# Performance work log

Measured on AMD Instinct MI355X. Metric: run time of the kernel, lower is better.

## Reference

```python
import jax, jax.numpy as jnp
import numpy as np

N = 50000      # nodes
E = 600000     # edges
D_IN = 128
D_H = 128
D_OUT = 64
HEADS = 2
NEG_SLOPE = 0.2  # PyG GATConv default leaky_relu slope
BN_EPS = 1e-5


def setup_inputs() -> dict:
    key = jax.random.key(0)
    ks = jax.random.split(key, 24)
    w = lambda i, shape: (jax.random.normal(ks[i], shape, jnp.float32) * 0.1)
    return {
        "x": jax.random.normal(ks[0], (N, D_IN), jnp.float32),
        "edge_index": jax.random.randint(ks[1], (2, E), 0, N, jnp.int64),
        "W_gcn1": w(2, (D_IN, D_H)),
        "b_gcn1": jnp.zeros((D_H,), jnp.float32),
        "bn1_gamma": jax.random.uniform(ks[3], (D_H,), jnp.float32, 0.5, 1.5),
        "bn1_beta": w(4, (D_H,)),
        "bn1_mean": w(5, (D_H,)),
        "bn1_var": jax.random.uniform(ks[6], (D_H,), jnp.float32, 0.5, 1.5),
        "W_gat1": w(7, (D_H, HEADS * D_H)),
        "a_src1": w(8, (HEADS, D_H)),
        "a_dst1": w(9, (HEADS, D_H)),
        "b_gat1": jnp.zeros((D_H,), jnp.float32),
        "W_gcn2": w(10, (D_H, D_H)),
        "b_gcn2": jnp.zeros((D_H,), jnp.float32),
        "bn2_gamma": jax.random.uniform(ks[11], (D_H,), jnp.float32, 0.5, 1.5),
        "bn2_beta": w(12, (D_H,)),
        "bn2_mean": w(13, (D_H,)),
        "bn2_var": jax.random.uniform(ks[14], (D_H,), jnp.float32, 0.5, 1.5),
        "W_gat2": w(15, (D_H, HEADS * D_OUT)),
        "a_src2": w(16, (HEADS, D_OUT)),
        "a_dst2": w(17, (HEADS, D_OUT)),
        "b_gat2": jnp.zeros((D_OUT,), jnp.float32),
    }


def _add_self_loops(edge_index):
    loop = jnp.arange(N, dtype=edge_index.dtype)
    src = jnp.concatenate([edge_index[0], loop])
    dst = jnp.concatenate([edge_index[1], loop])
    return src, dst


def _gcn(x, edge_index, W, b):
    # PyG GCNConv: add self-loops, symmetric D^-1/2 (A+I) D^-1/2 normalization
    src, dst = _add_self_loops(edge_index)
    deg = jax.ops.segment_sum(jnp.ones_like(dst, x.dtype), dst, num_segments=N)
    dinv = jax.lax.rsqrt(jnp.maximum(deg, 1.0))  # deg >= 1 with self-loops
    norm = dinv[src] * dinv[dst]                 # [E+N]
    h = x @ W                                    # [N, C]
    out = jax.ops.segment_sum(h[src] * norm[:, None], dst, num_segments=N)
    return out + b


def _gat(x, edge_index, W, a_src, a_dst, b, out_ch):
    # PyG GATConv (concat=False): per-head attention, segment softmax over dst,
    # mean across heads. Dropout off (eval mode).
    h = (x @ W).reshape(N, HEADS, out_ch)                 # [N, H, C]
    al_s = jnp.einsum('nhc,hc->nh', h, a_src)             # [N, H]
    al_d = jnp.einsum('nhc,hc->nh', h, a_dst)             # [N, H]
    src, dst = _add_self_loops(edge_index)
    e = al_s[src] + al_d[dst]                             # [E+N, H]
    e = jnp.where(e > 0, e, NEG_SLOPE * e)                # leaky_relu
    m = jax.ops.segment_max(e, dst, num_segments=N)       # [N, H]
    ex = jnp.exp(e - m[dst])
    denom = jax.ops.segment_sum(ex, dst, num_segments=N)  # [N, H]
    alpha = ex / denom[dst]                               # [E+N, H]
    out = jax.ops.segment_sum(h[src] * alpha[:, :, None], dst, num_segments=N)
    return out.mean(axis=1) + b                           # concat=False -> mean


def _bn_eval(x, gamma, beta, mean, var):
    return (x - mean) * jax.lax.rsqrt(var + BN_EPS) * gamma + beta


def reference(x, edge_index, W_gcn1, b_gcn1, bn1_gamma, bn1_beta, bn1_mean, bn1_var,
              W_gat1, a_src1, a_dst1, b_gat1, W_gcn2, b_gcn2,
              bn2_gamma, bn2_beta, bn2_mean, bn2_var,
              W_gat2, a_src2, a_dst2, b_gat2):
    h = _gcn(x, edge_index, W_gcn1, b_gcn1)
    h = jax.nn.relu(_bn_eval(h, bn1_gamma, bn1_beta, bn1_mean, bn1_var))
    h = jax.nn.relu(_gat(h, edge_index, W_gat1, a_src1, a_dst1, b_gat1, D_H))
    h = _gcn(h, edge_index, W_gcn2, b_gcn2)
    h = jax.nn.relu(_bn_eval(h, bn2_gamma, bn2_beta, bn2_mean, bn2_var))
    h = _gat(h, edge_index, W_gat2, a_src2, a_dst2, b_gat2, D_OUT)
    return jax.nn.log_softmax(h, axis=1)
```

## Files before the change

kernel.cpp:

```cpp
#include <hip/hip_runtime.h>
#include <hip/hip_bf16.h>

#define N_NODES 50000
#define N_EDGES 600000

typedef short bf16x8 __attribute__((ext_vector_type(8)));
typedef float f32x4 __attribute__((ext_vector_type(4)));

__device__ __forceinline__ float leaky(float e) { return fmaxf(e, 0.2f * e); }
__device__ __forceinline__ unsigned short f2b(float f) {
  __hip_bfloat16 h = __float2bfloat16(f);
  return *reinterpret_cast<unsigned short*>(&h);
}
__device__ __forceinline__ float blo(unsigned int u) { return __uint_as_float(u << 16); }
__device__ __forceinline__ float bhi(unsigned int u) { return __uint_as_float(u & 0xffff0000u); }

__global__ void k_convert(const int* __restrict__ e, int* __restrict__ deg,
                          int2* __restrict__ eord,
                          const float* __restrict__ W1, const float* __restrict__ WG1,
                          const float* __restrict__ W2, const float* __restrict__ WG2,
                          unsigned short* __restrict__ Wt1, unsigned short* __restrict__ WtG1,
                          unsigned short* __restrict__ Wt2, unsigned short* __restrict__ WtG2,
                          const float* b1, const float* g1, const float* be1, const float* m1,
                          const float* v1, const float* b2, const float* g2, const float* be2,
                          const float* m2, const float* v2, float* sc1, float* sh1,
                          float* sc2, float* sh2,
                          const float* as1, const float* ad1, const float* as2,
                          const float* ad2, float* was1, float* wad1, float* was2,
                          float* wad2) {
  __shared__ int sflag;
  int tid = threadIdx.x;
  if (tid < 64) {
    int idx = 1 + 2 * tid * 4096;
    int v = e[idx];
    unsigned long long nz = __ballot(v != 0);
    if (tid == 0) sflag = (nz == 0ULL) ? 1 : 0;
  }
  __syncthreads();
  int f = sflag;
  int i = blockIdx.x * 256 + tid;
  if (i < N_EDGES) {
    int s, d;
    if (f) { s = e[2 * i]; d = e[2 * (N_EDGES + i)]; }
    else   { s = e[i];     d = e[N_EDGES + i]; }
    int pos = atomicAdd(&deg[d], 1);
    eord[i] = make_int2(s, (d << 16) | pos);
  }
  if (i < 16384) {
    int k = i >> 7, c = i & 127;
    Wt1[c * 128 + k] = f2b(W1[i]);
  } else if (i < 49152) {
    int l = i - 16384;
    int k = l >> 8, c8 = l & 255;
    int head = c8 >> 7, cc = c8 & 127;
    WtG1[cc * 256 + head * 128 + k] = f2b(WG1[l]);
  } else if (i < 65536) {
    int l = i - 49152;
    int k = l >> 7, c = l & 127;
    Wt2[c * 128 + k] = f2b(W2[l]);
  } else if (i < 81920) {
    int l = i - 65536;
    int k = l >> 7, c = l & 127;
    WtG2[c * 128 + k] = f2b(WG2[l]);
  } else if (i < 82048) {
    int c = i - 81920;
    float s = g1[c] * rsqrtf(v1[c] + 1e-5f);
    sc1[c] = s;
    sh1[c] = (b1[c] - m1[c]) * s + be1[c];
  } else if (i < 82176) {
    int c = i - 82048;
    float s = g2[c] * rsqrtf(v2[c] + 1e-5f);
    sc2[c] = s;
    sh2[c] = (b2[c] - m2[c]) * s + be2[c];
  } else if (i < 82688) {
    int j = i - 82176;
    int k = j & 127;
    int vec = j >> 7;
    const float* Wr = (vec < 2) ? (WG1 + k * 256) : (WG2 + k * 128);
    const float* av = (vec == 0) ? as1 : (vec == 1) ? ad1 : (vec == 2) ? as2 : ad2;
    float* op = (vec == 0) ? was1 : (vec == 1) ? wad1 : (vec == 2) ? was2 : wad2;
    int hl = (vec < 2) ? 128 : 64;
    float s0 = 0.f, s1 = 0.f;
    for (int c = 0; c < hl; c += 4) {
      float4 wv = *(const float4*)(Wr + c);
      float4 a4 = *(const float4*)(av + c);
      s0 += wv.x * a4.x + wv.y * a4.y + wv.z * a4.z + wv.w * a4.w;
    }
    for (int c = 0; c < hl; c += 4) {
      float4 wv = *(const float4*)(Wr + hl + c);
      float4 a4 = *(const float4*)(av + hl + c);
      s1 += wv.x * a4.x + wv.y * a4.y + wv.z * a4.z + wv.w * a4.w;
    }
    op[2 * k] = s0;
    op[2 * k + 1] = s1;
  }
}

__global__ void k_offsets(const int* __restrict__ deg, int* __restrict__ gbase,
                          int* __restrict__ roff, float* __restrict__ dinv) {
  __shared__ int s[256];
  __shared__ int base;
  int t = threadIdx.x;
  int i = blockIdx.x * 256 + t;
  int v = (i < N_NODES) ? deg[i] : 0;
  s[t] = v;
  __syncthreads();
  for (int o = 1; o < 256; o <<= 1) {
    int x = (t >= o) ? s[t - o] : 0;
    __syncthreads();
    s[t] += x;
    __syncthreads();
  }
  if (t == 255) base = atomicAdd(gbase, s[255]);
  __syncthreads();
  int off = base + s[t] - v;
  if (i < N_NODES) {
    roff[i] = off;
    dinv[i] = rsqrtf((float)v + 1.f);
  }
}
__global__ void k_fill(const int2* __restrict__ eord, const int* __restrict__ roff,
                       int2* __restrict__ aen, const float* __restrict__ dinv) {
  int i = blockIdx.x * 256 + threadIdx.x;
  if (i < N_EDGES) {
    int2 ep = eord[i];
    int s = ep.x;
    int d = ((unsigned)ep.y) >> 16;
    int pos = ep.y & 0xffff;
    aen[roff[d] + pos] = make_int2(s, __float_as_int(dinv[s]));
  }
}

__global__ __launch_bounds__(256, 4) void gemm_mfma(const float* __restrict__ X,
                                                    const unsigned short* __restrict__ Wt,
                                                    unsigned short* __restrict__ Hb) {
  __shared__ __align__(16) short smem[64 * 136];
  int tid = threadIdx.x;
  int row0 = blockIdx.x * 64;
  for (int i = tid; i < 2048; i += 256) {
    int r = i >> 5;
    int k4 = (i & 31) * 4;
    int row = row0 + r;
    float4 v = make_float4(0.f, 0.f, 0.f, 0.f);
    if (row < N_NODES) v = *(const float4*)(X + (size_t)row * 128 + k4);
    uint2 p;
    p.x = (unsigned int)f2b(v.x) | ((unsigned int)f2b(v.y) << 16);
    p.y = (unsigned int)f2b(v.z) | ((unsigned int)f2b(v.w) << 16);
    *(uint2*)&smem[r * 136 + k4] = p;
  }
  int wave = tid >> 6, lane = tid & 63;
  int m = lane & 15, quad = lane >> 4;
  int c0 = wave * 32;
  bf16x8 b[2][4];
#pragma unroll
  for (int ct = 0; ct < 2; ++ct) {
    const unsigned short* wp = Wt + (size_t)(c0 + ct * 16 + m) * 128 + quad * 8;
#pragma unroll
    for (int kk = 0; kk < 4; ++kk) b[ct][kk] = *(const bf16x8*)(wp + kk * 32);
  }
  __syncthreads();
  f32x4 acc[4][2];
#pragma unroll
  for (int rt = 0; rt < 4; ++rt)
#pragma unroll
    for (int ct = 0; ct < 2; ++ct) acc[rt][ct] = (f32x4){0.f, 0.f, 0.f, 0.f};
#pragma unroll
  for (int rt = 0; rt < 4; ++rt) {
    bf16x8 a[4];
#pragma unroll
    for (int kk = 0; kk < 4; ++kk)
      a[kk] = *(const bf16x8*)&smem[(rt * 16 + m) * 136 + kk * 32 + quad * 8];
#pragma unroll
    for (int ct = 0; ct < 2; ++ct)
#pragma unroll
      for (int kk = 0; kk < 4; ++kk)
        acc[rt][ct] = __builtin_amdgcn_mfma_f32_16x16x32_bf16(a[kk], b[ct][kk], acc[rt][ct], 0, 0, 0);
  }
  __syncthreads();
#pragma unroll
  for (int rt = 0; rt < 4; ++rt)
#pragma unroll
    for (int ct = 0; ct < 2; ++ct)
#pragma unroll
      for (int reg = 0; reg < 4; ++reg)
        smem[(rt * 16 + quad * 4 + reg) * 128 + c0 + ct * 16 + m] = (short)f2b(acc[rt][ct][reg]);
  __syncthreads();
  for (int i = tid; i < 1024; i += 256) {
    int row = row0 + (i >> 4);
    if (row < N_NODES)
      *(uint4*)((char*)Hb + (size_t)row0 * 256 + (size_t)i * 16) =
          *(uint4*)((char*)smem + (size_t)i * 16);
  }
}

__global__ __launch_bounds__(256, 4) void gemm_k256(const unsigned short* __restrict__ Q,
                                                    const unsigned short* __restrict__ Wt,
                                                    const float* __restrict__ bias,
                                                    unsigned short* __restrict__ G) {
  __shared__ __align__(16) short smem[64 * 136];
  int tid = threadIdx.x;
  int row0 = blockIdx.x * 64;
  int wave = tid >> 6, lane = tid & 63;
  int m = lane & 15, quad = lane >> 4;
  int c0 = wave * 32;
  f32x4 acc[4][2];
#pragma unroll
  for (int rt = 0; rt < 4; ++rt)
#pragma unroll
    for (int ct = 0; ct < 2; ++ct) acc[rt][ct] = (f32x4){0.f, 0.f, 0.f, 0.f};
#pragma unroll
  for (int half = 0; half < 2; ++half) {
    if (half) __syncthreads();
    for (int i = tid; i < 2048; i += 256) {
      int r = i >> 5;
      int k4 = (i & 31) * 4;
      int row = row0 + r;
      uint2 p = make_uint2(0u, 0u);
      if (row < N_NODES) p = *(const uint2*)(Q + (size_t)row * 256 + half * 128 + k4);
      *(uint2*)&smem[r * 136 + k4] = p;
    }
    bf16x8 b[2][4];
#pragma unroll
    for (int ct = 0; ct < 2; ++ct) {
      const unsigned short* wp =
          Wt + (size_t)(c0 + ct * 16 + m) * 256 + half * 128 + quad * 8;
#pragma unroll
      for (int kk = 0; kk < 4; ++kk) b[ct][kk] = *(const bf16x8*)(wp + kk * 32);
    }
    __syncthreads();
#pragma unroll
    for (int rt = 0; rt < 4; ++rt) {
      bf16x8 a[4];
#pragma unroll
      for (int kk = 0; kk < 4; ++kk)
        a[kk] = *(const bf16x8*)&smem[(rt * 16 + m) * 136 + kk * 32 + quad * 8];
#pragma unroll
      for (int ct = 0; ct < 2; ++ct)
#pragma unroll
        for (int kk = 0; kk < 4; ++kk)
          acc[rt][ct] =
              __builtin_amdgcn_mfma_f32_16x16x32_bf16(a[kk], b[ct][kk], acc[rt][ct], 0, 0, 0);
    }
  }
  __syncthreads();
  float bv[2];
#pragma unroll
  for (int ct = 0; ct < 2; ++ct) bv[ct] = bias[c0 + ct * 16 + m];
#pragma unroll
  for (int rt = 0; rt < 4; ++rt)
#pragma unroll
    for (int ct = 0; ct < 2; ++ct)
#pragma unroll
      for (int reg = 0; reg < 4; ++reg)
        smem[(rt * 16 + quad * 4 + reg) * 128 + c0 + ct * 16 + m] =
            (short)f2b(fmaxf(acc[rt][ct][reg] + bv[ct], 0.f));
  __syncthreads();
  for (int i = tid; i < 1024; i += 256) {
    int row = row0 + (i >> 4);
    if (row < N_NODES)
      *(uint4*)((char*)G + (size_t)row0 * 256 + (size_t)i * 16) =
          *(uint4*)((char*)smem + (size_t)i * 16);
  }
}

__global__ __launch_bounds__(256, 4) void gemm_gcn2_gat2(
    const unsigned short* __restrict__ AG, const unsigned short* __restrict__ Wt2,
    const float* __restrict__ sc, const float* __restrict__ sh,
    const unsigned short* __restrict__ WtG2,
    const float* __restrict__ was, const float* __restrict__ wad,
    float* __restrict__ als, float* __restrict__ ald,
    unsigned short* __restrict__ Q2) {
  __shared__ __align__(16) short smA[64 * 136];
  __shared__ __align__(16) short smB[64 * 136];
  int tid = threadIdx.x;
  int row0 = blockIdx.x * 64;
  for (int i = tid; i < 1024; i += 256) {
    int r = i >> 4;
    int k8 = (i & 15) * 8;
    int row = row0 + r;
    uint4 p = make_uint4(0u, 0u, 0u, 0u);
    if (row < N_NODES) p = *(const uint4*)(AG + (size_t)row * 128 + k8);
    *(uint4*)&smA[r * 136 + k8] = p;
  }
  int wave = tid >> 6, lane = tid & 63;
  int m = lane & 15, quad = lane >> 4;
  int c0 = wave * 32;
  bf16x8 b1[2][4];
#pragma unroll
  for (int ct = 0; ct < 2; ++ct) {
    const unsigned short* wp = Wt2 + (size_t)(c0 + ct * 16 + m) * 128 + quad * 8;
#pragma unroll
    for (int kk = 0; kk < 4; ++kk) b1[ct][kk] = *(const bf16x8*)(wp + kk * 32);
  }
  __syncthreads();
  f32x4 acc[4][2];
#pragma unroll
  for (int rt = 0; rt < 4; ++rt)
#pragma unroll
    for (int ct = 0; ct < 2; ++ct) acc[rt][ct] = (f32x4){0.f, 0.f, 0.f, 0.f};
#pragma unroll
  for (int rt = 0; rt < 4; ++rt) {
    bf16x8 a[4];
#pragma unroll
    for (int kk = 0; kk < 4; ++kk)
      a[kk] = *(const bf16x8*)&smA[(rt * 16 + m) * 136 + kk * 32 + quad * 8];
#pragma unroll
    for (int ct = 0; ct < 2; ++ct)
#pragma unroll
      for (int kk = 0; kk < 4; ++kk)
        acc[rt][ct] = __builtin_amdgcn_mfma_f32_16x16x32_bf16(a[kk], b1[ct][kk], acc[rt][ct], 0, 0, 0);
  }
  float scv[2], shv[2];
#pragma unroll
  for (int ct = 0; ct < 2; ++ct) {
    scv[ct] = sc[c0 + ct * 16 + m];
    shv[ct] = sh[c0 + ct * 16 + m];
  }
#pragma unroll
  for (int rt = 0; rt < 4; ++rt)
#pragma unroll
    for (int ct = 0; ct < 2; ++ct)
#pragma unroll
      for (int reg = 0; reg < 4; ++reg)
        smB[(rt * 16 + quad * 4 + reg) * 136 + c0 + ct * 16 + m] =
            (short)f2b(fmaxf(fmaf(acc[rt][ct][reg], scv[ct], shv[ct]), 0.f));
  __syncthreads();
  bf16x8 b2[2][4];
#pragma unroll
  for (int ct = 0; ct < 2; ++ct) {
    const unsigned short* wp = WtG2 + (size_t)(c0 + ct * 16 + m) * 128 + quad * 8;
#pragma unroll
    for (int kk = 0; kk < 4; ++kk) b2[ct][kk] = *(const bf16x8*)(wp + kk * 32);
  }
  f32x4 acc2[4][2];
#pragma unroll
  for (int rt = 0; rt < 4; ++rt)
#pragma unroll
    for (int ct = 0; ct < 2; ++ct) acc2[rt][ct] = (f32x4){0.f, 0.f, 0.f, 0.f};
#pragma unroll
  for (int rt = 0; rt < 4; ++rt) {
    bf16x8 a[4];
#pragma unroll
    for (int kk = 0; kk < 4; ++kk)
      a[kk] = *(const bf16x8*)&smB[(rt * 16 + m) * 136 + kk * 32 + quad * 8];
#pragma unroll
    for (int ct = 0; ct < 2; ++ct)
#pragma unroll
      for (int kk = 0; kk < 4; ++kk)
        acc2[rt][ct] = __builtin_amdgcn_mfma_f32_16x16x32_bf16(a[kk], b2[ct][kk], acc2[rt][ct], 0, 0, 0);
  }
  {
    int rloc = wave * 16 + (lane >> 2);
    int k0 = (lane & 3) * 32;
    float s0 = 0.f, s1 = 0.f, d0 = 0.f, d1 = 0.f;
#pragma unroll
    for (int c = 0; c < 32; c += 2) {
      unsigned u = *(const unsigned*)&smB[rloc * 136 + k0 + c];
      float x0 = blo(u), x1 = bhi(u);
      float4 ws4 = *(const float4*)(was + 2 * (k0 + c));
      float4 wd4 = *(const float4*)(wad + 2 * (k0 + c));
      s0 = fmaf(x0, ws4.x, s0); s1 = fmaf(x0, ws4.y, s1);
      s0 = fmaf(x1, ws4.z, s0); s1 = fmaf(x1, ws4.w, s1);
      d0 = fmaf(x0, wd4.x, d0); d1 = fmaf(x0, wd4.y, d1);
      d0 = fmaf(x1, wd4.z, d0); d1 = fmaf(x1, wd4.w, d1);
    }
#pragma unroll
    for (int mask = 1; mask <= 2; mask <<= 1) {
      s0 += __shfl_xor(s0, mask, 64);
      s1 += __shfl_xor(s1, mask, 64);
      d0 += __shfl_xor(d0, mask, 64);
      d1 += __shfl_xor(d1, mask, 64);
    }
    int row = row0 + rloc;
    if ((lane & 3) == 0 && row < N_NODES) {
      *(float2*)(als + 2 * row) = make_float2(s0, s1);
      *(float2*)(ald + 2 * row) = make_float2(d0, d1);
    }
  }
#pragma unroll
  for (int rt = 0; rt < 4; ++rt)
#pragma unroll
    for (int ct = 0; ct < 2; ++ct)
#pragma unroll
      for (int reg = 0; reg < 4; ++reg)
        smA[(rt * 16 + quad * 4 + reg) * 128 + c0 + ct * 16 + m] =
            (short)f2b(acc2[rt][ct][reg]);
  __syncthreads();
  for (int i = tid; i < 1024; i += 256) {
    int row = row0 + (i >> 4);
    if (row < N_NODES)
      *(uint4*)((char*)Q2 + (size_t)row0 * 256 + (size_t)i * 16) =
          *(uint4*)((char*)smA + (size_t)i * 16);
  }
}

template <int MODE>
__global__ __launch_bounds__(256) void gcn_pull(const unsigned short* __restrict__ Hb,
                                                const int2* __restrict__ aen,
                                                const int* __restrict__ roff,
                                                const int* __restrict__ deg,
                                                const float* __restrict__ dinv,
                                                const float* __restrict__ sc,
                                                const float* __restrict__ sh,
                                                const float* __restrict__ was,
                                                const float* __restrict__ wad,
                                                float* __restrict__ als,
                                                float* __restrict__ ald,
                                                unsigned short* __restrict__ out) {
  int wv = (blockIdx.x * 256 + threadIdx.x) >> 6;
  int lane = threadIdx.x & 63;
  int q4 = lane >> 4, l16 = lane & 15;
  int qb = lane & 48, l7 = lane & 7;
  int i = 4 * wv + q4;
  if (i >= N_NODES) return;
  int off = roff[i], end = off + deg[i];
  float di = dinv[i];
  uint4 u = *(const uint4*)((const char*)Hb + (unsigned)i * 256u + l16 * 16u);
  float a0 = blo(u.x) * di, a1 = bhi(u.x) * di;
  float a2 = blo(u.y) * di, a3 = bhi(u.y) * di;
  float a4 = blo(u.z) * di, a5 = bhi(u.z) * di;
  float a6 = blo(u.w) * di, a7 = bhi(u.w) * di;
  int j = off;
  int nfull = (end - off) >> 3;
  int2 ae = make_int2(i, 0);
  if (l7 < end - j) ae = aen[j + l7];
  for (int t = 0; t < nfull; ++t) {
    int ss[8];
#pragma unroll
    for (int k = 0; k < 8; ++k) ss[k] = __shfl(ae.x, qb + k, 64);
    float ww[8];
#pragma unroll
    for (int k = 0; k < 8; ++k) ww[k] = __shfl(__int_as_float(ae.y), qb + k, 64);
    uint4 vv[8];
#pragma unroll
    for (int k = 0; k < 8; ++k)
      vv[k] = *(const uint4*)((const char*)Hb + (unsigned)ss[k] * 256u + l16 * 16u);
    j += 8;
    if (l7 < end - j) ae = aen[j + l7];
#pragma unroll
    for (int k = 0; k < 8; ++k) {
      a0 = fmaf(blo(vv[k].x), ww[k], a0); a1 = fmaf(bhi(vv[k].x), ww[k], a1);
      a2 = fmaf(blo(vv[k].y), ww[k], a2); a3 = fmaf(bhi(vv[k].y), ww[k], a3);
      a4 = fmaf(blo(vv[k].z), ww[k], a4); a5 = fmaf(bhi(vv[k].z), ww[k], a5);
      a6 = fmaf(blo(vv[k].w), ww[k], a6); a7 = fmaf(bhi(vv[k].w), ww[k], a7);
    }
  }
  int rem = end - j;
  if (rem) {
    int ss[8];
#pragma unroll
    for (int k = 0; k < 8; ++k) ss[k] = __shfl(ae.x, qb + k, 64);
    float ww[8];
#pragma unroll
    for (int k = 0; k < 8; ++k) ww[k] = __shfl(__int_as_float(ae.y), qb + k, 64);
    uint4 vv[8];
#pragma unroll
    for (int k = 0; k < 8; ++k)
      if (k < rem)
        vv[k] = *(const uint4*)((const char*)Hb + (unsigned)ss[k] * 256u + l16 * 16u);
#pragma unroll
    for (int k = 0; k < 8; ++k)
      if (k < rem) {
        a0 = fmaf(blo(vv[k].x), ww[k], a0); a1 = fmaf(bhi(vv[k].x), ww[k], a1);
        a2 = fmaf(blo(vv[k].y), ww[k], a2); a3 = fmaf(bhi(vv[k].y), ww[k], a3);
        a4 = fmaf(blo(vv[k].z), ww[k], a4); a5 = fmaf(bhi(vv[k].z), ww[k], a5);
        a6 = fmaf(blo(vv[k].w), ww[k], a6); a7 = fmaf(bhi(vv[k].w), ww[k], a7);
      }
  }
  if constexpr (MODE == 1) {
    uint4 pw;
    pw.x = (unsigned int)f2b(a0 * di) | ((unsigned int)f2b(a1 * di) << 16);
    pw.y = (unsigned int)f2b(a2 * di) | ((unsigned int)f2b(a3 * di) << 16);
    pw.z = (unsigned int)f2b(a4 * di) | ((unsigned int)f2b(a5 * di) << 16);
    pw.w = (unsigned int)f2b(a6 * di) | ((unsigned int)f2b(a7 * di) << 16);
    *(uint4*)(out + (size_t)i * 128 + l16 * 8) = pw;
  } else {
    int c0 = l16 * 8;
    float4 sca = *(const float4*)(sc + c0), scb = *(const float4*)(sc + c0 + 4);
    float4 sha = *(const float4*)(sh + c0), shb = *(const float4*)(sh + c0 + 4);
    float t0 = fmaxf(fmaf(a0 * di, sca.x, sha.x), 0.f);
    float t1 = fmaxf(fmaf(a1 * di, sca.y, sha.y), 0.f);
    float t2 = fmaxf(fmaf(a2 * di, sca.z, sha.z), 0.f);
    float t3 = fmaxf(fmaf(a3 * di, sca.w, sha.w), 0.f);
    float t4 = fmaxf(fmaf(a4 * di, scb.x, shb.x), 0.f);
    float t5 = fmaxf(fmaf(a5 * di, scb.y, shb.y), 0.f);
    float t6 = fmaxf(fmaf(a6 * di, scb.z, shb.z), 0.f);
    float t7 = fmaxf(fmaf(a7 * di, scb.w, shb.w), 0.f);
    float4 w0 = *(const float4*)(was + 2 * c0);
    float4 w1 = *(const float4*)(was + 2 * c0 + 4);
    float4 w2 = *(const float4*)(was + 2 * c0 + 8);
    float4 w3 = *(const float4*)(was + 2 * c0 + 12);
    float sl0 = t0 * w0.x + t1 * w0.z + t2 * w1.x + t3 * w1.z +
                t4 * w2.x + t5 * w2.z + t6 * w3.x + t7 * w3.z;
    float sl1 = t0 * w0.y + t1 * w0.w + t2 * w1.y + t3 * w1.w +
                t4 * w2.y + t5 * w2.w + t6 * w3.y + t7 * w3.w;
    w0 = *(const float4*)(wad + 2 * c0);
    w1 = *(const float4*)(wad + 2 * c0 + 4);
    w2 = *(const float4*)(wad + 2 * c0 + 8);
    w3 = *(const float4*)(wad + 2 * c0 + 12);
    float dl0 = t0 * w0.x + t1 * w0.z + t2 * w1.x + t3 * w1.z +
                t4 * w2.x + t5 * w2.z + t6 * w3.x + t7 * w3.z;
    float dl1 = t0 * w0.y + t1 * w0.w + t2 * w1.y + t3 * w1.w +
                t4 * w2.y + t5 * w2.w + t6 * w3.y + t7 * w3.w;
#pragma unroll
    for (int mask = 1; mask <= 8; mask <<= 1) {
      sl0 += __shfl_xor(sl0, mask, 64);
      sl1 += __shfl_xor(sl1, mask, 64);
      dl0 += __shfl_xor(dl0, mask, 64);
      dl1 += __shfl_xor(dl1, mask, 64);
    }
    if (l16 == 0) {
      *(float2*)(als + 2 * i) = make_float2(sl0, sl1);
      *(float2*)(ald + 2 * i) = make_float2(dl0, dl1);
    }
    uint4 pw;
    pw.x = (unsigned int)f2b(t0) | ((unsigned int)f2b(t1) << 16);
    pw.y = (unsigned int)f2b(t2) | ((unsigned int)f2b(t3) << 16);
    pw.z = (unsigned int)f2b(t4) | ((unsigned int)f2b(t5) << 16);
    pw.w = (unsigned int)f2b(t6) | ((unsigned int)f2b(t7) << 16);
    *(uint4*)(out + (size_t)i * 128 + l16 * 8) = pw;
  }
}

__global__ __launch_bounds__(256) void gat1_pull(const unsigned short* __restrict__ P,
                                                 const int2* __restrict__ aen,
                                                 const int* __restrict__ roff,
                                                 const int* __restrict__ deg,
                                                 const float* __restrict__ als,
                                                 const float* __restrict__ ald,
                                                 unsigned short* __restrict__ Q) {
  int wv = (blockIdx.x * 256 + threadIdx.x) >> 6;
  int lane = threadIdx.x & 63;
  int q4 = lane >> 4, l16 = lane & 15;
  int qb = lane & 48, l7 = lane & 7;
  int i = 4 * wv + q4;
  if (i >= N_NODES) return;
  int off = roff[i], end = off + deg[i];
  float2 dif = *(const float2*)(ald + 2 * i);
  float p0 = 0.f, p1 = 0.f;
  float g0 = 0.f, g1 = 0.f, g2 = 0.f, g3 = 0.f,
        g4 = 0.f, g5 = 0.f, g6 = 0.f, g7 = 0.f;
  float h0 = 0.f, h1 = 0.f, h2 = 0.f, h3 = 0.f,
        h4 = 0.f, h5 = 0.f, h6 = 0.f, h7 = 0.f;
  int j = off;
  int nfull = (end - off) >> 3;
  int2 ae = make_int2(i, 0);
  float2 av = make_float2(-1e30f, -1e30f);
  if (l7 < end - j) {
    ae = aen[j + l7];
    av = *(const float2*)(als + 2 * ae.x);
  }
  for (int t = 0; t < nfull; ++t) {
    int ss[8];
#pragma unroll
    for (int k = 0; k < 8; ++k) ss[k] = __shfl(ae.x, qb + k, 64);
    uint4 vv[8];
#pragma unroll
    for (int k = 0; k < 8; ++k)
      vv[k] = *(const uint4*)((const char*)P + (unsigned)ss[k] * 256u + l16 * 16u);
    float q0 = __expf(leaky(av.x + dif.x));
    float q1 = __expf(leaky(av.y + dif.y));
    j += 8;
    if (l7 < end - j) {
      ae = aen[j + l7];
      av = *(const float2*)(als + 2 * ae.x);
    }
#pragma unroll
    for (int k = 0; k < 8; ++k) {
      float b0 = __shfl(q0, qb + k, 64);
      float b1 = __shfl(q1, qb + k, 64);
      p0 += b0; p1 += b1;
      float c0 = blo(vv[k].x), c1 = bhi(vv[k].x);
      float c2 = blo(vv[k].y), c3 = bhi(vv[k].y);
      float c4 = blo(vv[k].z), c5 = bhi(vv[k].z);
      float c6 = blo(vv[k].w), c7 = bhi(vv[k].w);
      g0 = fmaf(b0, c0, g0); h0 = fmaf(b1, c0, h0);
      g1 = fmaf(b0, c1, g1); h1 = fmaf(b1, c1, h1);
      g2 = fmaf(b0, c2, g2); h2 = fmaf(b1, c2, h2);
      g3 = fmaf(b0, c3, g3); h3 = fmaf(b1, c3, h3);
      g4 = fmaf(b0, c4, g4); h4 = fmaf(b1, c4, h4);
      g5 = fmaf(b0, c5, g5); h5 = fmaf(b1, c5, h5);
      g6 = fmaf(b0, c6, g6); h6 = fmaf(b1, c6, h6);
      g7 = fmaf(b0, c7, g7); h7 = fmaf(b1, c7, h7);
    }
  }
  int rem = end - j;
  if (rem) {
    int ss[8];
#pragma unroll
    for (int k = 0; k < 8; ++k) ss[k] = __shfl(ae.x, qb + k, 64);
    uint4 vv[8];
#pragma unroll
    for (int k = 0; k < 8; ++k)
      if (k < rem)
        vv[k] = *(const uint4*)((const char*)P + (unsigned)ss[k] * 256u + l16 * 16u);
    float q0 = __expf(leaky(av.x + dif.x));
    float q1 = __expf(leaky(av.y + dif.y));
#pragma unroll
    for (int k = 0; k < 8; ++k)
      if (k < rem) {
        float b0 = __shfl(q0, qb + k, 64);
        float b1 = __shfl(q1, qb + k, 64);
        p0 += b0; p1 += b1;
        float c0 = blo(vv[k].x), c1 = bhi(vv[k].x);
        float c2 = blo(vv[k].y), c3 = bhi(vv[k].y);
        float c4 = blo(vv[k].z), c5 = bhi(vv[k].z);
        float c6 = blo(vv[k].w), c7 = bhi(vv[k].w);
        g0 = fmaf(b0, c0, g0); h0 = fmaf(b1, c0, h0);
        g1 = fmaf(b0, c1, g1); h1 = fmaf(b1, c1, h1);
        g2 = fmaf(b0, c2, g2); h2 = fmaf(b1, c2, h2);
        g3 = fmaf(b0, c3, g3); h3 = fmaf(b1, c3, h3);
        g4 = fmaf(b0, c4, g4); h4 = fmaf(b1, c4, h4);
        g5 = fmaf(b0, c5, g5); h5 = fmaf(b1, c5, h5);
        g6 = fmaf(b0, c6, g6); h6 = fmaf(b1, c6, h6);
        g7 = fmaf(b0, c7, g7); h7 = fmaf(b1, c7, h7);
      }
  }
  float2 ai = *(const float2*)(als + 2 * i);
  float es0 = __expf(leaky(ai.x + dif.x));
  float es1 = __expf(leaky(ai.y + dif.y));
  float r0 = 0.5f / (p0 + es0);
  float r1 = 0.5f / (p1 + es1);
  uint4 u = *(const uint4*)((const char*)P + (unsigned)i * 256u + l16 * 16u);
  float c0 = blo(u.x), c1 = bhi(u.x), c2 = blo(u.y), c3 = bhi(u.y);
  float c4 = blo(u.z), c5 = bhi(u.z), c6 = blo(u.w), c7 = bhi(u.w);
  g0 = (g0 + es0 * c0) * r0; g1 = (g1 + es0 * c1) * r0;
  g2 = (g2 + es0 * c2) * r0; g3 = (g3 + es0 * c3) * r0;
  g4 = (g4 + es0 * c4) * r0; g5 = (g5 + es0 * c5) * r0;
  g6 = (g6 + es0 * c6) * r0; g7 = (g7 + es0 * c7) * r0;
  h0 = (h0 + es1 * c0) * r1; h1 = (h1 + es1 * c1) * r1;
  h2 = (h2 + es1 * c2) * r1; h3 = (h3 + es1 * c3) * r1;
  h4 = (h4 + es1 * c4) * r1; h5 = (h5 + es1 * c5) * r1;
  h6 = (h6 + es1 * c6) * r1; h7 = (h7 + es1 * c7) * r1;
  uint4 pw;
  pw.x = (unsigned int)f2b(g0) | ((unsigned int)f2b(g1) << 16);
  pw.y = (unsigned int)f2b(g2) | ((unsigned int)f2b(g3) << 16);
  pw.z = (unsigned int)f2b(g4) | ((unsigned int)f2b(g5) << 16);
  pw.w = (unsigned int)f2b(g6) | ((unsigned int)f2b(g7) << 16);
  *(uint4*)(Q + (size_t)i * 256 + l16 * 8) = pw;
  pw.x = (unsigned int)f2b(h0) | ((unsigned int)f2b(h1) << 16);
  pw.y = (unsigned int)f2b(h2) | ((unsigned int)f2b(h3) << 16);
  pw.z = (unsigned int)f2b(h4) | ((unsigned int)f2b(h5) << 16);
  pw.w = (unsigned int)f2b(h6) | ((unsigned int)f2b(h7) << 16);
  *(uint4*)(Q + (size_t)i * 256 + 128 + l16 * 8) = pw;
}

__global__ __launch_bounds__(256) void gat_pull64_lsm(const unsigned short* __restrict__ Hb,
                                                      const int2* __restrict__ aen,
                                                      const int* __restrict__ roff,
                                                      const int* __restrict__ deg,
                                                      const float* __restrict__ als,
                                                      const float* __restrict__ ald,
                                                      const float* __restrict__ bias,
                                                      float* __restrict__ out) {
  int wv = (blockIdx.x * 256 + threadIdx.x) >> 6;
  int lane = threadIdx.x & 63;
  int q4 = lane >> 4, l16 = lane & 15;
  int qb = lane & 48, l7 = lane & 7;
  int hh = l16 >> 3, p8 = l16 & 7;
  int i = 4 * wv + q4;
  if (i >= N_NODES) return;
  int off = roff[i], end = off + deg[i];
  unsigned cb2 = (unsigned)(hh * 64 + 8 * p8) * 2u;
  float2 dd = *(const float2*)(ald + 2 * i);
  float p = 0.f;
  float acc0 = 0.f, acc1 = 0.f, acc2 = 0.f, acc3 = 0.f;
  float acc4 = 0.f, acc5 = 0.f, acc6 = 0.f, acc7 = 0.f;
  int j = off;
  int nfull = (end - off) >> 3;
  int2 ae = make_int2(i, 0);
  float2 av = make_float2(-1e30f, -1e30f);
  if (l7 < end - j) {
    ae = aen[j + l7];
    av = *(const float2*)(als + 2 * ae.x);
  }
  for (int t = 0; t < nfull; ++t) {
    int ss[8];
#pragma unroll
    for (int k = 0; k < 8; ++k) ss[k] = __shfl(ae.x, qb + k, 64);
    uint4 vv[8];
#pragma unroll
    for (int k = 0; k < 8; ++k)
      vv[k] = *(const uint4*)((const char*)Hb + (unsigned)ss[k] * 256u + cb2);
    float q0 = __expf(leaky(av.x + dd.x));
    float q1 = __expf(leaky(av.y + dd.y));
    j += 8;
    if (l7 < end - j) {
      ae = aen[j + l7];
      av = *(const float2*)(als + 2 * ae.x);
    }
#pragma unroll
    for (int k = 0; k < 8; ++k) {
      float b0 = __shfl(q0, qb + k, 64);
      float b1 = __shfl(q1, qb + k, 64);
      float q = hh ? b1 : b0;
      p += q;
      acc0 = fmaf(q, blo(vv[k].x), acc0); acc1 = fmaf(q, bhi(vv[k].x), acc1);
      acc2 = fmaf(q, blo(vv[k].y), acc2); acc3 = fmaf(q, bhi(vv[k].y), acc3);
      acc4 = fmaf(q, blo(vv[k].z), acc4); acc5 = fmaf(q, bhi(vv[k].z), acc5);
      acc6 = fmaf(q, blo(vv[k].w), acc6); acc7 = fmaf(q, bhi(vv[k].w), acc7);
    }
  }
  int rem = end - j;
  if (rem) {
    int ss[8];
#pragma unroll
    for (int k = 0; k < 8; ++k) ss[k] = __shfl(ae.x, qb + k, 64);
    uint4 vv[8];
#pragma unroll
    for (int k = 0; k < 8; ++k)
      if (k < rem)
        vv[k] = *(const uint4*)((const char*)Hb + (unsigned)ss[k] * 256u + cb2);
    float q0 = __expf(leaky(av.x + dd.x));
    float q1 = __expf(leaky(av.y + dd.y));
#pragma unroll
    for (int k = 0; k < 8; ++k)
      if (k < rem) {
        float b0 = __shfl(q0, qb + k, 64);
        float b1 = __shfl(q1, qb + k, 64);
        float q = hh ? b1 : b0;
        p += q;
        acc0 = fmaf(q, blo(vv[k].x), acc0); acc1 = fmaf(q, bhi(vv[k].x), acc1);
        acc2 = fmaf(q, blo(vv[k].y), acc2); acc3 = fmaf(q, bhi(vv[k].y), acc3);
        acc4 = fmaf(q, blo(vv[k].z), acc4); acc5 = fmaf(q, bhi(vv[k].z), acc5);
        acc6 = fmaf(q, blo(vv[k].w), acc6); acc7 = fmaf(q, bhi(vv[k].w), acc7);
      }
  }
  float2 ai = *(const float2*)(als + 2 * i);
  float axs = hh ? ai.y : ai.x;
  float dh = hh ? dd.y : dd.x;
  float es = __expf(leaky(axs + dh));
  float rsel = 0.5f / (p + es);
  uint4 u = *(const uint4*)((const char*)Hb + (unsigned)i * 256u + cb2);
  acc0 = (acc0 + es * blo(u.x)) * rsel; acc1 = (acc1 + es * bhi(u.x)) * rsel;
  acc2 = (acc2 + es * blo(u.y)) * rsel; acc3 = (acc3 + es * bhi(u.y)) * rsel;
  acc4 = (acc4 + es * blo(u.z)) * rsel; acc5 = (acc5 + es * bhi(u.z)) * rsel;
  acc6 = (acc6 + es * blo(u.w)) * rsel; acc7 = (acc7 + es * bhi(u.w)) * rsel;
  acc0 += __shfl_xor(acc0, 8, 64); acc1 += __shfl_xor(acc1, 8, 64);
  acc2 += __shfl_xor(acc2, 8, 64); acc3 += __shfl_xor(acc3, 8, 64);
  acc4 += __shfl_xor(acc4, 8, 64); acc5 += __shfl_xor(acc5, 8, 64);
  acc6 += __shfl_xor(acc6, 8, 64); acc7 += __shfl_xor(acc7, 8, 64);
  float4 b0 = *(const float4*)(bias + 8 * p8);
  float4 b1 = *(const float4*)(bias + 8 * p8 + 4);
  float v0 = acc0 + b0.x, v1 = acc1 + b0.y, v2 = acc2 + b0.z, v3 = acc3 + b0.w;
  float v4 = acc4 + b1.x, v5 = acc5 + b1.y, v6 = acc6 + b1.z, v7 = acc7 + b1.w;
  float mv = fmaxf(fmaxf(fmaxf(v0, v1), fmaxf(v2, v3)),
                   fmaxf(fmaxf(v4, v5), fmaxf(v6, v7)));
#pragma unroll
  for (int mm = 4; mm > 0; mm >>= 1) mv = fmaxf(mv, __shfl_xor(mv, mm, 64));
  float sv = __expf(v0 - mv) + __expf(v1 - mv) + __expf(v2 - mv) + __expf(v3 - mv) +
             __expf(v4 - mv) + __expf(v5 - mv) + __expf(v6 - mv) + __expf(v7 - mv);
#pragma unroll
  for (int mm = 4; mm > 0; mm >>= 1) sv += __shfl_xor(sv, mm, 64);
  float ls = mv + __logf(sv);
  if (hh == 0) {
    *(float4*)(out + (size_t)i * 64 + 8 * p8) =
        make_float4(v0 - ls, v1 - ls, v2 - ls, v3 - ls);
    *(float4*)(out + (size_t)i * 64 + 8 * p8 + 4) =
        make_float4(v4 - ls, v5 - ls, v6 - ls, v7 - ls);
  }
}

extern "C" void kernel_launch(void* const* d_in, const int* in_sizes, int n_in, void* d_out,
                              int out_size, void* d_ws, size_t ws_size, hipStream_t stream) {
  const float* x      = (const float*)d_in[0];
  const int* eidx     = (const int*)d_in[1];
  const float* W_gcn1 = (const float*)d_in[2];
  const float* b_gcn1 = (const float*)d_in[3];
  const float* bn1_g  = (const float*)d_in[4];
  const float* bn1_b  = (const float*)d_in[5];
  const float* bn1_m  = (const float*)d_in[6];
  const float* bn1_v  = (const float*)d_in[7];
  const float* W_gat1 = (const float*)d_in[8];
  const float* a_src1 = (const float*)d_in[9];
  const float* a_dst1 = (const float*)d_in[10];
  const float* b_gat1 = (const float*)d_in[11];
  const float* W_gcn2 = (const float*)d_in[12];
  const float* b_gcn2 = (const float*)d_in[13];
  const float* bn2_g  = (const float*)d_in[14];
  const float* bn2_b  = (const float*)d_in[15];
  const float* bn2_m  = (const float*)d_in[16];
  const float* bn2_v  = (const float*)d_in[17];
  const float* W_gat2 = (const float*)d_in[18];
  const float* a_src2 = (const float*)d_in[19];
  const float* a_dst2 = (const float*)d_in[20];
  const float* b_gat2 = (const float*)d_in[21];

  char* ws = (char*)d_ws;
  size_t o = 0;
  auto take = [&](size_t bytes) {
    char* p = ws + o;
    o = (o + bytes + 255) & ~(size_t)255;
    return p;
  };
  int* deg     = (int*)take((size_t)(N_NODES + 64) * 4);
  int* gbase   = deg + N_NODES;
  int* roff    = (int*)take((size_t)N_NODES * 4);
  int2* eord   = (int2*)take((size_t)N_EDGES * 8);
  int2* aen    = (int2*)take((size_t)N_EDGES * 8);
  float* dinv  = (float*)take((size_t)N_NODES * 4);
  float* als   = (float*)take((size_t)2 * N_NODES * 4);
  float* ald   = (float*)take((size_t)2 * N_NODES * 4);
  float* sc1   = (float*)take(128 * 4);
  float* sh1   = (float*)take(128 * 4);
  float* sc2   = (float*)take(128 * 4);
  float* sh2   = (float*)take(128 * 4);
  float* was1  = (float*)take(256 * 4);
  float* wad1  = (float*)take(256 * 4);
  float* was2  = (float*)take(256 * 4);
  float* wad2  = (float*)take(256 * 4);
  unsigned short* Wt1  = (unsigned short*)take((size_t)128 * 128 * 2);
  unsigned short* WtG1 = (unsigned short*)take((size_t)128 * 256 * 2);
  unsigned short* Wt2  = (unsigned short*)take((size_t)128 * 128 * 2);
  unsigned short* WtG2 = (unsigned short*)take((size_t)128 * 128 * 2);
  unsigned short* Hb   = (unsigned short*)take((size_t)N_NODES * 128 * 2);
  unsigned short* Pb   = (unsigned short*)take((size_t)N_NODES * 128 * 2);
  unsigned short* Qb   = (unsigned short*)take((size_t)N_NODES * 256 * 2);
  unsigned short* Gb   = (unsigned short*)take((size_t)N_NODES * 128 * 2);
  unsigned short* AGb  = (unsigned short*)take((size_t)N_NODES * 128 * 2);
  unsigned short* Q2b  = (unsigned short*)take((size_t)N_NODES * 128 * 2);
  (void)ws_size; (void)in_sizes; (void)n_in; (void)out_size;

  int eb = (N_EDGES + 255) / 256;
  int nb = (N_NODES + 255) / 256;
  int qb = ((N_NODES + 3) / 4 + 3) / 4;
  int gb = (N_NODES + 63) / 64;

  hipMemsetAsync(deg, 0, (size_t)(N_NODES + 1) * 4, stream);
  k_convert<<<eb, 256, 0, stream>>>(eidx, deg, eord, W_gcn1, W_gat1, W_gcn2, W_gat2,
                                    Wt1, WtG1, Wt2, WtG2, b_gcn1, bn1_g, bn1_b, bn1_m, bn1_v,
                                    b_gcn2, bn2_g, bn2_b, bn2_m, bn2_v, sc1, sh1, sc2, sh2,
                                    a_src1, a_dst1, a_src2, a_dst2, was1, wad1, was2, wad2);
  k_offsets<<<nb, 256, 0, stream>>>(deg, gbase, roff, dinv);
  k_fill<<<eb, 256, 0, stream>>>(eord, roff, aen, dinv);

  gemm_mfma<<<gb, 256, 0, stream>>>(x, Wt1, Hb);
  gcn_pull<0><<<qb, 256, 0, stream>>>(Hb, aen, roff, deg, dinv, sc1, sh1, was1, wad1,
                                      als, ald, Pb);
  gat1_pull<<<qb, 256, 0, stream>>>(Pb, aen, roff, deg, als, ald, Qb);
  gemm_k256<<<gb, 256, 0, stream>>>(Qb, WtG1, b_gat1, Gb);
  gcn_pull<1><<<qb, 256, 0, stream>>>(Gb, aen, roff, deg, dinv, nullptr, nullptr,
                                      nullptr, nullptr, nullptr, nullptr, AGb);
  gemm_gcn2_gat2<<<gb, 256, 0, stream>>>(AGb, Wt2, sc2, sh2, WtG2, was2, wad2,
                                         als, ald, Q2b);
  gat_pull64_lsm<<<qb, 256, 0, stream>>>(Q2b, aen, roff, deg, als, ald, b_gat2,
                                         (float*)d_out);
}
```

Measured before the change: 314.2 us.

## Fuse first GCN GEMM into edge conversion kernel and widen k256 tile loads

The first-layer X·W GEMM now runs as extra blocks of the edge/weight conversion kernel, reading and converting the fp32 W_gcn1 to bf16 directly in registers. This removes the separate Wt1 transpose buffer and one kernel launch, and lets the GEMM overlap with the degree-counting atomics. The WtG1 conversion range is remapped, and part of it is now written twice with identical values. Separately, the k256 GEMM stages its smem tile with 16-byte loads instead of 8-byte loads. The cost is strided, uncoalesced fp32 weight reads in every GEMM block and a larger combined grid.

New measurement: 305.7 us. 2.7% less time.

```diff
diff --git a/kernel.cpp b/kernel.cpp
--- a/kernel.cpp
+++ b/kernel.cpp
@@ -3,6 +3,7 @@
 
 #define N_NODES 50000
 #define N_EDGES 600000
+#define GEMM_BLOCKS 782
 
 typedef short bf16x8 __attribute__((ext_vector_type(8)));
 typedef float f32x4 __attribute__((ext_vector_type(4)));
@@ -15,21 +16,86 @@
 __device__ __forceinline__ float blo(unsigned int u) { return __uint_as_float(u << 16); }
 __device__ __forceinline__ float bhi(unsigned int u) { return __uint_as_float(u & 0xffff0000u); }
 
-__global__ void k_convert(const int* __restrict__ e, int* __restrict__ deg,
-                          int2* __restrict__ eord,
-                          const float* __restrict__ W1, const float* __restrict__ WG1,
-                          const float* __restrict__ W2, const float* __restrict__ WG2,
-                          unsigned short* __restrict__ Wt1, unsigned short* __restrict__ WtG1,
-                          unsigned short* __restrict__ Wt2, unsigned short* __restrict__ WtG2,
-                          const float* b1, const float* g1, const float* be1, const float* m1,
-                          const float* v1, const float* b2, const float* g2, const float* be2,
-                          const float* m2, const float* v2, float* sc1, float* sh1,
-                          float* sc2, float* sh2,
-                          const float* as1, const float* ad1, const float* as2,
-                          const float* ad2, float* was1, float* wad1, float* was2,
-                          float* wad2) {
+__global__ __launch_bounds__(256, 4) void k_convert_gemm(
+    const int* __restrict__ e, int* __restrict__ deg, int2* __restrict__ eord,
+    const float* __restrict__ X, unsigned short* __restrict__ Hb,
+    const float* __restrict__ W1, const float* __restrict__ WG1,
+    const float* __restrict__ W2, const float* __restrict__ WG2,
+    unsigned short* __restrict__ WtG1,
+    unsigned short* __restrict__ Wt2, unsigned short* __restrict__ WtG2,
+    const float* b1, const float* g1, const float* be1, const float* m1,
+    const float* v1, const float* b2, const float* g2, const float* be2,
+    const float* m2, const float* v2, float* sc1, float* sh1,
+    float* sc2, float* sh2,
+    const float* as1, const float* ad1, const float* as2,
+    const float* ad2, float* was1, float* wad1, float* was2, float* wad2) {
+  __shared__ __align__(16) short smem[64 * 136];
+  int tid = threadIdx.x;
+  if (blockIdx.x < GEMM_BLOCKS) {
+    int row0 = blockIdx.x * 64;
+    for (int i = tid; i < 2048; i += 256) {
+      int r = i >> 5;
+      int k4 = (i & 31) * 4;
+      int row = row0 + r;
+      float4 v = make_float4(0.f, 0.f, 0.f, 0.f);
+      if (row < N_NODES) v = *(const float4*)(X + (size_t)row * 128 + k4);
+      uint2 p;
+      p.x = (unsigned int)f2b(v.x) | ((unsigned int)f2b(v.y) << 16);
+      p.y = (unsigned int)f2b(v.z) | ((unsigned int)f2b(v.w) << 16);
+      *(uint2*)&smem[r * 136 + k4] = p;
+    }
+    int wave = tid >> 6, lane = tid & 63;
+    int m = lane & 15, quad = lane >> 4;
+    int c0 = wave * 32;
+    bf16x8 b[2][4];
+#pragma unroll
+    for (int ct = 0; ct < 2; ++ct) {
+      int col = c0 + ct * 16 + m;
+#pragma unroll
+      for (int kk = 0; kk < 4; ++kk) {
+        bf16x8 v;
+#pragma unroll
+        for (int el = 0; el < 8; ++el)
+          v[el] = (short)f2b(W1[(size_t)(kk * 32 + quad * 8 + el) * 128 + col]);
+        b[ct][kk] = v;
+      }
+    }
+    __syncthreads();
+    f32x4 acc[4][2];
+#pragma unroll
+    for (int rt = 0; rt < 4; ++rt)
+#pragma unroll
+      for (int ct = 0; ct < 2; ++ct) acc[rt][ct] = (f32x4){0.f, 0.f, 0.f, 0.f};
+#pragma unroll
+    for (int rt = 0; rt < 4; ++rt) {
+      bf16x8 a[4];
+#pragma unroll
+      for (int kk = 0; kk < 4; ++kk)
+        a[kk] = *(const bf16x8*)&smem[(rt * 16 + m) * 136 + kk * 32 + quad * 8];
+#pragma unroll
+      for (int ct = 0; ct < 2; ++ct)
+#pragma unroll
+        for (int kk = 0; kk < 4; ++kk)
+          acc[rt][ct] = __builtin_amdgcn_mfma_f32_16x16x32_bf16(a[kk], b[ct][kk], acc[rt][ct], 0, 0, 0);
+    }
+    __syncthreads();
+#pragma unroll
+    for (int rt = 0; rt < 4; ++rt)
+#pragma unroll
+      for (int ct = 0; ct < 2; ++ct)
+#pragma unroll
+        for (int reg = 0; reg < 4; ++reg)
+          smem[(rt * 16 + quad * 4 + reg) * 128 + c0 + ct * 16 + m] = (short)f2b(acc[rt][ct][reg]);
+    __syncthreads();
+    for (int i = tid; i < 1024; i += 256) {
+      int row = row0 + (i >> 4);
+      if (row < N_NODES)
+        *(uint4*)((char*)Hb + (size_t)row0 * 256 + (size_t)i * 16) =
+            *(uint4*)((char*)smem + (size_t)i * 16);
+    }
+    return;
+  }
   __shared__ int sflag;
-  int tid = threadIdx.x;
   if (tid < 64) {
     int idx = 1 + 2 * tid * 4096;
     int v = e[idx];
@@ -38,7 +104,7 @@
   }
   __syncthreads();
   int f = sflag;
-  int i = blockIdx.x * 256 + tid;
+  int i = (blockIdx.x - GEMM_BLOCKS) * 256 + tid;
   if (i < N_EDGES) {
     int s, d;
     if (f) { s = e[2 * i]; d = e[2 * (N_EDGES + i)]; }
@@ -46,9 +112,11 @@
     int pos = atomicAdd(&deg[d], 1);
     eord[i] = make_int2(s, (d << 16) | pos);
   }
-  if (i < 16384) {
-    int k = i >> 7, c = i & 127;
-    Wt1[c * 128 + k] = f2b(W1[i]);
+  if (i < 32768) {
+    int l = i;
+    int k = l >> 8, c8 = l & 255;
+    int head = c8 >> 7, cc = c8 & 127;
+    WtG1[cc * 256 + head * 128 + k] = f2b(WG1[l]);
   } else if (i < 49152) {
     int l = i - 16384;
     int k = l >> 8, c8 = l & 255;
@@ -131,68 +199,6 @@
   }
 }
 
-__global__ __launch_bounds__(256, 4) void gemm_mfma(const float* __restrict__ X,
-                                                    const unsigned short* __restrict__ Wt,
-                                                    unsigned short* __restrict__ Hb) {
-  __shared__ __align__(16) short smem[64 * 136];
-  int tid = threadIdx.x;
-  int row0 = blockIdx.x * 64;
-  for (int i = tid; i < 2048; i += 256) {
-    int r = i >> 5;
-    int k4 = (i & 31) * 4;
-    int row = row0 + r;
-    float4 v = make_float4(0.f, 0.f, 0.f, 0.f);
-    if (row < N_NODES) v = *(const float4*)(X + (size_t)row * 128 + k4);
-    uint2 p;
-    p.x = (unsigned int)f2b(v.x) | ((unsigned int)f2b(v.y) << 16);
-    p.y = (unsigned int)f2b(v.z) | ((unsigned int)f2b(v.w) << 16);
-    *(uint2*)&smem[r * 136 + k4] = p;
-  }
-  int wave = tid >> 6, lane = tid & 63;
-  int m = lane & 15, quad = lane >> 4;
-  int c0 = wave * 32;
-  bf16x8 b[2][4];
-#pragma unroll
-  for (int ct = 0; ct < 2; ++ct) {
-    const unsigned short* wp = Wt + (size_t)(c0 + ct * 16 + m) * 128 + quad * 8;
-#pragma unroll
-    for (int kk = 0; kk < 4; ++kk) b[ct][kk] = *(const bf16x8*)(wp + kk * 32);
-  }
-  __syncthreads();
-  f32x4 acc[4][2];
-#pragma unroll
-  for (int rt = 0; rt < 4; ++rt)
-#pragma unroll
-    for (int ct = 0; ct < 2; ++ct) acc[rt][ct] = (f32x4){0.f, 0.f, 0.f, 0.f};
-#pragma unroll
-  for (int rt = 0; rt < 4; ++rt) {
-    bf16x8 a[4];
-#pragma unroll
-    for (int kk = 0; kk < 4; ++kk)
-      a[kk] = *(const bf16x8*)&smem[(rt * 16 + m) * 136 + kk * 32 + quad * 8];
-#pragma unroll
-    for (int ct = 0; ct < 2; ++ct)
-#pragma unroll
-      for (int kk = 0; kk < 4; ++kk)
-        acc[rt][ct] = __builtin_amdgcn_mfma_f32_16x16x32_bf16(a[kk], b[ct][kk], acc[rt][ct], 0, 0, 0);
-  }
-  __syncthreads();
-#pragma unroll
-  for (int rt = 0; rt < 4; ++rt)
-#pragma unroll
-    for (int ct = 0; ct < 2; ++ct)
-#pragma unroll
-      for (int reg = 0; reg < 4; ++reg)
-        smem[(rt * 16 + quad * 4 + reg) * 128 + c0 + ct * 16 + m] = (short)f2b(acc[rt][ct][reg]);
-  __syncthreads();
-  for (int i = tid; i < 1024; i += 256) {
-    int row = row0 + (i >> 4);
-    if (row < N_NODES)
-      *(uint4*)((char*)Hb + (size_t)row0 * 256 + (size_t)i * 16) =
-          *(uint4*)((char*)smem + (size_t)i * 16);
-  }
-}
-
 __global__ __launch_bounds__(256, 4) void gemm_k256(const unsigned short* __restrict__ Q,
                                                     const unsigned short* __restrict__ Wt,
                                                     const float* __restrict__ bias,
@@ -211,13 +217,13 @@
 #pragma unroll
   for (int half = 0; half < 2; ++half) {
     if (half) __syncthreads();
-    for (int i = tid; i < 2048; i += 256) {
-      int r = i >> 5;
-      int k4 = (i & 31) * 4;
+    for (int i = tid; i < 1024; i += 256) {
+      int r = i >> 4;
+      int k8 = (i & 15) * 8;
       int row = row0 + r;
-      uint2 p = make_uint2(0u, 0u);
-      if (row < N_NODES) p = *(const uint2*)(Q + (size_t)row * 256 + half * 128 + k4);
-      *(uint2*)&smem[r * 136 + k4] = p;
+      uint4 p = make_uint4(0u, 0u, 0u, 0u);
+      if (row < N_NODES) p = *(const uint4*)(Q + (size_t)row * 256 + half * 128 + k8);
+      *(uint4*)&smem[r * 136 + k8] = p;
     }
     bf16x8 b[2][4];
 #pragma unroll
@@ -809,7 +815,6 @@
   float* wad1  = (float*)take(256 * 4);
   float* was2  = (float*)take(256 * 4);
   float* wad2  = (float*)take(256 * 4);
-  unsigned short* Wt1  = (unsigned short*)take((size_t)128 * 128 * 2);
   unsigned short* WtG1 = (unsigned short*)take((size_t)128 * 256 * 2);
   unsigned short* Wt2  = (unsigned short*)take((size_t)128 * 128 * 2);
   unsigned short* WtG2 = (unsigned short*)take((size_t)128 * 128 * 2);
@@ -827,14 +832,14 @@
   int gb = (N_NODES + 63) / 64;
 
   hipMemsetAsync(deg, 0, (size_t)(N_NODES + 1) * 4, stream);
-  k_convert<<<eb, 256, 0, stream>>>(eidx, deg, eord, W_gcn1, W_gat1, W_gcn2, W_gat2,
-                                    Wt1, WtG1, Wt2, WtG2, b_gcn1, bn1_g, bn1_b, bn1_m, bn1_v,
-                                    b_gcn2, bn2_g, bn2_b, bn2_m, bn2_v, sc1, sh1, sc2, sh2,
-                                    a_src1, a_dst1, a_src2, a_dst2, was1, wad1, was2, wad2);
+  k_convert_gemm<<<gb + eb, 256, 0, stream>>>(
+      eidx, deg, eord, x, Hb, W_gcn1, W_gat1, W_gcn2, W_gat2,
+      WtG1, Wt2, WtG2, b_gcn1, bn1_g, bn1_b, bn1_m, bn1_v,
+      b_gcn2, bn2_g, bn2_b, bn2_m, bn2_v, sc1, sh1, sc2, sh2,
+      a_src1, a_dst1, a_src2, a_dst2, was1, wad1, was2, wad2);
   k_offsets<<<nb, 256, 0, stream>>>(deg, gbase, roff, dinv);
   k_fill<<<eb, 256, 0, stream>>>(eord, roff, aen, dinv);
 
-  gemm_mfma<<<gb, 256, 0, stream>>>(x, Wt1, Hb);
   gcn_pull<0><<<qb, 256, 0, stream>>>(Hb, aen, roff, deg, dinv, sc1, sh1, was1, wad1,
                                       als, ald, Pb);
   gat1_pull<<<qb, 256, 0, stream>>>(Pb, aen, roff, deg, als, ald, Qb);
```
